# Kernel tuning notes

Measured on AMD Instinct MI355X. Metric: run time of the kernel, lower is better.

The kernel has to match this reference:

```python
import jax, jax.numpy as jnp
import numpy as np

DIM = 2048
N_HEADS = 16
N_KV = 4
HEAD_DIM = DIM // N_HEADS  # 128
B, S = 2, 2048
EPS = float(np.finfo(np.float32).eps)  # torch RMSNorm eps=None -> finfo eps


def _rotate_half(x):
    # interleaved-pair rotation: out[..., ::2] = -x[..., 1::2]; out[..., 1::2] = x[..., ::2]
    x2 = x.reshape(x.shape[:-1] + (HEAD_DIM // 2, 2))
    rot = jnp.stack([-x2[..., 1], x2[..., 0]], axis=-1)
    return rot.reshape(x.shape)


def _rmsnorm(x, w):
    var = jnp.mean(x * x, axis=-1, keepdims=True)
    return x * jax.lax.rsqrt(var + EPS) * w


def setup_inputs() -> dict:
    key = jax.random.key(0)
    ks = jax.random.split(key, 5)
    out_f = (N_HEADS + 2 * N_KV) * HEAD_DIM  # 3072
    return {
        "x": jax.random.normal(ks[0], (B, S, DIM), jnp.float32),
        "wqkv": jax.random.normal(ks[1], (out_f, DIM), jnp.float32) * (2.0 / (DIM + out_f)) ** 0.5,
        "wo": jax.random.normal(ks[2], (DIM, DIM), jnp.float32) * (1.0 / DIM) ** 0.5,
        "q_norm_w": jnp.ones((HEAD_DIM,), jnp.float32),
        "k_norm_w": jnp.ones((HEAD_DIM,), jnp.float32),
        "freqs_cos": jnp.cos(jax.random.normal(ks[3], (S, 1, HEAD_DIM), jnp.float32)),
        "freqs_sin": jnp.sin(jax.random.normal(ks[4], (S, 1, HEAD_DIM), jnp.float32)),
    }


def reference(x, wqkv, wo, q_norm_w, k_norm_w, freqs_cos, freqs_sin):
    b, s, _ = x.shape
    qkv = jnp.einsum("bsd,od->bso", x, wqkv)
    q_size = N_HEADS * HEAD_DIM
    kv_size = N_KV * HEAD_DIM
    xq = qkv[..., :q_size].reshape(b, s, N_HEADS, HEAD_DIM)
    xk = qkv[..., q_size:q_size + kv_size].reshape(b, s, N_KV, HEAD_DIM)
    xv = qkv[..., q_size + kv_size:].reshape(b, s, N_KV, HEAD_DIM)
    xq = _rmsnorm(xq, q_norm_w)
    xk = _rmsnorm(xk, k_norm_w)
    # RoPE (freqs broadcast over batch and heads)
    xq = xq * freqs_cos + _rotate_half(xq) * freqs_sin
    xk = xk * freqs_cos + _rotate_half(xk) * freqs_sin
    # GQA: group query heads per kv head instead of materializing repeats
    rep = N_HEADS // N_KV
    q = xq.transpose(0, 2, 1, 3).reshape(b, N_KV, rep, s, HEAD_DIM)
    k = xk.transpose(0, 2, 1, 3)  # [b, kv, s, d]
    v = xv.transpose(0, 2, 1, 3)
    scale = 1.0 / jnp.sqrt(jnp.asarray(HEAD_DIM, x.dtype))
    scores = jnp.einsum("bhgqd,bhkd->bhgqk", q, k) * scale
    probs = jax.nn.softmax(scores, axis=-1)
    attn = jnp.einsum("bhgqk,bhkd->bhgqd", probs, v)
    attn = attn.reshape(b, N_HEADS, s, HEAD_DIM).transpose(0, 2, 1, 3).reshape(b, s, DIM)
    return jnp.einsum("bsd,od->bso", attn, wo)
```

## Files before the change

### kernel.cpp

```cpp
#include <hip/hip_runtime.h>

typedef unsigned short u16;
typedef __bf16 bf16x8 __attribute__((ext_vector_type(8)));
typedef u16 u16x8 __attribute__((ext_vector_type(8)));
typedef float f32x4 __attribute__((ext_vector_type(4)));
typedef float f32x16 __attribute__((ext_vector_type(16)));

__device__ __forceinline__ u16 f2bf(float f) {
    unsigned u = __float_as_uint(f);
    return (u16)((u + 0x7fffu + ((u >> 16) & 1u)) >> 16);
}
__device__ __forceinline__ unsigned pk2(float a, float b) {
    return (unsigned)f2bf(a) | ((unsigned)f2bf(b) << 16);
}

__global__ void cvt_bf16(const float* __restrict__ src, u16* __restrict__ dst, int n4) {
    int i = blockIdx.x * 256 + threadIdx.x;
    if (i >= n4) return;
    float4 v = *(const float4*)(src + (size_t)i * 4);
    uint2 o; o.x = pk2(v.x, v.y); o.y = pk2(v.z, v.w);
    *(uint2*)(dst + (size_t)i * 4) = o;
}

__global__ __launch_bounds__(256)
void gemm_bt(const u16* __restrict__ A, const u16* __restrict__ B,
             float* __restrict__ C, int M, int N, int K) {
    __shared__ u16 As[128 * 32];
    __shared__ u16 Bs[128 * 32];
    const int tid = threadIdx.x;
    const int wave = tid >> 6, lane = tid & 63;
    const int quad = lane >> 4, l16 = lane & 15;
    const size_t bm = (size_t)blockIdx.y * 128;
    const size_t bn = (size_t)blockIdx.x * 128;
    const int wr = (wave >> 1) * 64;
    const int wc = (wave & 1) * 64;

    f32x4 acc[4][4] = {};

    const u16* Ab = A + bm * K;
    const u16* Bb = B + bn * K;
    const int strow = wave * 32 + (lane >> 2);
    const int stk = (lane & 3) * 8;

    for (int k0 = 0; k0 < K; k0 += 32) {
        __syncthreads();
#pragma unroll
        for (int c = 0; c < 2; ++c) {
            const u16* ga = Ab + (size_t)(strow + c * 16) * K + k0 + stk;
            const u16* gb = Bb + (size_t)(strow + c * 16) * K + k0 + stk;
            __builtin_amdgcn_global_load_lds(
                (__attribute__((address_space(1))) void*)ga,
                (__attribute__((address_space(3))) void*)&As[(wave * 32 + c * 16) * 32],
                16, 0, 0);
            __builtin_amdgcn_global_load_lds(
                (__attribute__((address_space(1))) void*)gb,
                (__attribute__((address_space(3))) void*)&Bs[(wave * 32 + c * 16) * 32],
                16, 0, 0);
        }
        __syncthreads();
        bf16x8 af[4], bfr[4];
#pragma unroll
        for (int mt = 0; mt < 4; ++mt)
            af[mt] = *(const bf16x8*)&As[(wr + mt * 16 + l16) * 32 + quad * 8];
#pragma unroll
        for (int nt = 0; nt < 4; ++nt)
            bfr[nt] = *(const bf16x8*)&Bs[(wc + nt * 16 + l16) * 32 + quad * 8];
#pragma unroll
        for (int mt = 0; mt < 4; ++mt)
#pragma unroll
            for (int nt = 0; nt < 4; ++nt)
                acc[mt][nt] = __builtin_amdgcn_mfma_f32_16x16x32_bf16(
                    af[mt], bfr[nt], acc[mt][nt], 0, 0, 0);
    }
#pragma unroll
    for (int mt = 0; mt < 4; ++mt)
#pragma unroll
        for (int nt = 0; nt < 4; ++nt)
#pragma unroll
            for (int r = 0; r < 4; ++r)
                C[(bm + wr + mt * 16 + quad * 4 + r) * (size_t)N + bn + wc + nt * 16 + l16] =
                    acc[mt][nt][r];
}

__global__ __launch_bounds__(256)
void normrope(const float* __restrict__ qkv, const float* __restrict__ qw,
              const float* __restrict__ kw, const float* __restrict__ fcos,
              const float* __restrict__ fsin, u16* __restrict__ qb, u16* __restrict__ kb) {
    int gw = blockIdx.x * 4 + (threadIdx.x >> 6);
    int lane = threadIdx.x & 63;
    int row = gw / 20;
    int task = gw - row * 20;
    int s = row & 2047;
    int b = row >> 11;
    const float* src;
    const float* w;
    u16* dst;
    float scl;
    if (task < 16) {
        src = qkv + (size_t)row * 3072 + task * 128;
        w = qw;
        dst = qb + ((size_t)(b * 16 + task) * 2048 + s) * 128;
        scl = 0.08838834764831845f * 1.4426950408889634f;
    } else {
        int kh = task - 16;
        src = qkv + (size_t)row * 3072 + 2048 + kh * 128;
        w = kw;
        dst = kb + ((size_t)(b * 4 + kh) * 2048 + s) * 128;
        scl = 1.0f;
    }
    float2 x = *(const float2*)(src + lane * 2);
    float ss = x.x * x.x + x.y * x.y;
#pragma unroll
    for (int off = 32; off >= 1; off >>= 1) ss += __shfl_xor(ss, off);
    float r = rsqrtf(ss * (1.0f / 128.0f) + 1.1920928955078125e-07f) * scl;
    float y0 = x.x * r * w[lane * 2];
    float y1 = x.y * r * w[lane * 2 + 1];
    float c0 = fcos[(size_t)s * 128 + lane * 2], c1 = fcos[(size_t)s * 128 + lane * 2 + 1];
    float s0 = fsin[(size_t)s * 128 + lane * 2], s1 = fsin[(size_t)s * 128 + lane * 2 + 1];
    dst[lane * 2]     = f2bf(y0 * c0 - y1 * s0);
    dst[lane * 2 + 1] = f2bf(y1 * c1 + y0 * s1);
}

__global__ __launch_bounds__(256)
void vtrans(const float* __restrict__ qkv, u16* __restrict__ vt) {
    __shared__ u16 tile[128 * 132];
    int blk = blockIdx.x;
    int kblk = blk & 15, kh = (blk >> 4) & 3, b = blk >> 6;
    int tid = threadIdx.x;
    const float* src = qkv + (size_t)(b * 2048 + kblk * 128) * 3072 + 2560 + kh * 128;
#pragma unroll
    for (int it = 0; it < 16; ++it) {
        int flat4 = tid + it * 256;
        int row = flat4 >> 5, c4 = flat4 & 31;
        float4 v = *(const float4*)(src + (size_t)row * 3072 + c4 * 4);
        u16* d = &tile[row * 132 + c4 * 4];
        d[0] = f2bf(v.x); d[1] = f2bf(v.y); d[2] = f2bf(v.z); d[3] = f2bf(v.w);
    }
    __syncthreads();
    int dd = tid >> 1, half = tid & 1;
    u16* dst = vt + ((size_t)(b * 4 + kh) * 128 + dd) * 2048 + kblk * 128 + half * 64;
#pragma unroll
    for (int k8 = 0; k8 < 8; ++k8) {
        u16x8 o;
#pragma unroll
        for (int j = 0; j < 8; ++j) o[j] = tile[(half * 64 + k8 * 8 + j) * 132 + dd];
        *(u16x8*)(dst + k8 * 8) = o;
    }
}

#define KBUF(c) ((c) * 8192)
#define VBUF(c) (16384 + (c) * 8192)
__global__ __launch_bounds__(256, 2)
void flash_attn(const u16* __restrict__ qb, const u16* __restrict__ kb,
                const u16* __restrict__ vt, u16* __restrict__ ab) {
    __shared__ u16 smem[32768];
    __shared__ float Llds[128];

    const int tid = threadIdx.x;
    const int wave = tid >> 6, lane = tid & 63;
    const int hf = lane >> 5, c32 = lane & 31;
    const int qt = blockIdx.x, hh = blockIdx.y, bb = blockIdx.z;
    const int kh = hh >> 2;

    const u16* Qbase = qb + (size_t)(bb * 16 + hh) * 2048 * 128;
    const u16* Kbase = kb + (size_t)(bb * 4 + kh) * 2048 * 128;
    const u16* Vbase = vt + (size_t)(bb * 4 + kh) * 128 * 2048;

    bf16x8 aq[8];
#pragma unroll
    for (int kq = 0; kq < 8; ++kq)
        aq[kq] = *(const bf16x8*)(Qbase +
            (size_t)(qt * 128 + wave * 32 + c32) * 128 + kq * 16 + hf * 8);

    f32x16 O[4] = {};
    float lacc = 0.f;

    const int st_key = tid >> 4, st_c16 = tid & 15;
    const int st_d = tid >> 3, st_c8 = tid & 7;

    u16x8 kreg[4], vreg[4];
#pragma unroll
    for (int it = 0; it < 4; ++it) {
        int key = st_key + it * 16, d = st_d + it * 32;
        kreg[it] = *(const u16x8*)(Kbase + (size_t)key * 128 + st_c16 * 8);
        vreg[it] = *(const u16x8*)(Vbase + (size_t)d * 2048 + st_c8 * 8);
    }
#pragma unroll
    for (int it = 0; it < 4; ++it) {
        int key = st_key + it * 16, d = st_d + it * 32;
        *(u16x8*)&smem[KBUF(0) + key * 128 + ((st_c16 ^ (key & 7)) * 8)] = kreg[it];
        *(u16x8*)&smem[VBUF(0) + d * 64 + ((st_c8 ^ (d & 7)) * 8)] = vreg[it];
    }
    __syncthreads();

    for (int kt = 0; kt < 32; ++kt) {
        const int cur = kt & 1, nxt = cur ^ 1;
        if (kt < 31) {
            const int key0n = (kt + 1) * 64;
#pragma unroll
            for (int it = 0; it < 4; ++it) {
                int key = st_key + it * 16, d = st_d + it * 32;
                kreg[it] = *(const u16x8*)(Kbase + (size_t)(key0n + key) * 128 + st_c16 * 8);
                vreg[it] = *(const u16x8*)(Vbase + (size_t)d * 2048 + key0n + st_c8 * 8);
            }
        }

        f32x16 sc[2] = {};
#pragma unroll
        for (int kq = 0; kq < 8; ++kq) {
#pragma unroll
            for (int mt = 0; mt < 2; ++mt) {
                bf16x8 kf = *(const bf16x8*)&smem[KBUF(cur) + (mt * 32 + c32) * 128 +
                                                 (((kq * 2 + hf) ^ (c32 & 7)) * 8)];
                sc[mt] = __builtin_amdgcn_mfma_f32_32x32x16_bf16(kf, aq[kq], sc[mt], 0, 0, 0);
            }
        }

        int pdw[2][8];
#pragma unroll
        for (int mt = 0; mt < 2; ++mt) {
            float p[16];
#pragma unroll
            for (int r = 0; r < 16; ++r) {
                p[r] = __builtin_amdgcn_exp2f(sc[mt][r]);
                lacc += p[r];
            }
#pragma unroll
            for (int i = 0; i < 8; ++i) pdw[mt][i] = (int)pk2(p[2 * i], p[2 * i + 1]);
        }

        if (kt < 31) {
#pragma unroll
            for (int it = 0; it < 4; ++it) {
                int key = st_key + it * 16, d = st_d + it * 32;
                *(u16x8*)&smem[KBUF(nxt) + key * 128 + ((st_c16 ^ (key & 7)) * 8)] = kreg[it];
                *(u16x8*)&smem[VBUF(nxt) + d * 64 + ((st_c8 ^ (d & 7)) * 8)] = vreg[it];
            }
        }

#pragma unroll
        for (int kc = 0; kc < 4; ++kc) {
            const int mt = kc >> 1, L = kc & 1;
            int s0 = hf ? pdw[mt][4 * L + 0] : pdw[mt][4 * L + 2];
            int s1 = hf ? pdw[mt][4 * L + 1] : pdw[mt][4 * L + 3];
            int r0 = __shfl_xor(s0, 32);
            int r1 = __shfl_xor(s1, 32);
            union { int i[4]; bf16x8 v; } u;
            u.i[0] = hf ? r0 : pdw[mt][4 * L + 0];
            u.i[1] = hf ? r1 : pdw[mt][4 * L + 1];
            u.i[2] = hf ? pdw[mt][4 * L + 2] : r0;
            u.i[3] = hf ? pdw[mt][4 * L + 3] : r1;
#pragma unroll
            for (int dt = 0; dt < 4; ++dt) {
                bf16x8 vf = *(const bf16x8*)&smem[VBUF(cur) + (dt * 32 + c32) * 64 +
                                                 (((kc * 2 + hf) ^ (c32 & 7)) * 8)];
                O[dt] = __builtin_amdgcn_mfma_f32_32x32x16_bf16(u.v, vf, O[dt], 0, 0, 0);
            }
        }
        __syncthreads();
    }

    float l = lacc + __shfl_xor(lacc, 32);
    if (hf == 0) Llds[wave * 32 + c32] = l;

    float inv[16];
#pragma unroll
    for (int r = 0; r < 16; ++r)
        inv[r] = __builtin_amdgcn_rcpf(Llds[wave * 32 + (r & 3) + 8 * (r >> 2) + 4 * hf]);

    u16* scr = &smem[wave * 32 * 136];
#pragma unroll
    for (int dt = 0; dt < 4; ++dt)
#pragma unroll
        for (int r = 0; r < 16; ++r) {
            int q_r = (r & 3) + 8 * (r >> 2) + 4 * hf;
            scr[q_r * 136 + dt * 32 + c32] = f2bf(O[dt][r] * inv[r]);
        }
#pragma unroll
    for (int it = 0; it < 8; ++it) {
        int f = it * 64 + lane;
        int row = f >> 4, c = f & 15;
        u16x8 v = *(const u16x8*)&scr[row * 136 + c * 8];
        int qg = qt * 128 + wave * 32 + row;
        *(u16x8*)(ab + ((size_t)(bb * 2048 + qg)) * 2048 + hh * 128 + c * 8) = v;
    }
}

extern "C" void kernel_launch(void* const* d_in, const int* in_sizes, int n_in,
                              void* d_out, int out_size, void* d_ws, size_t ws_size,
                              hipStream_t stream) {
    const float* x    = (const float*)d_in[0];
    const float* wqkv = (const float*)d_in[1];
    const float* wo   = (const float*)d_in[2];
    const float* qw   = (const float*)d_in[3];
    const float* kw   = (const float*)d_in[4];
    const float* fc   = (const float*)d_in[5];
    const float* fs   = (const float*)d_in[6];
    float* out = (float*)d_out;
    char* ws = (char*)d_ws;

    u16*   xb    = (u16*)(ws + 0);
    u16*   wqkvb = (u16*)(ws + 16777216);
    u16*   wob   = (u16*)(ws + 29360128);
    float* qkv   = (float*)(ws + 37748736);
    u16*   qb    = (u16*)(ws + 88080384);
    u16*   kb    = (u16*)(ws + 104857600);
    u16*   vt    = (u16*)(ws + 109051904);
    u16*   ab    = (u16*)(ws + 113246208);

    cvt_bf16<<<8192, 256, 0, stream>>>(x, xb, 2097152);
    cvt_bf16<<<6144, 256, 0, stream>>>(wqkv, wqkvb, 1572864);
    cvt_bf16<<<4096, 256, 0, stream>>>(wo, wob, 1048576);
    gemm_bt<<<dim3(24, 32), 256, 0, stream>>>(xb, wqkvb, qkv, 4096, 3072, 2048);
    normrope<<<20480, 256, 0, stream>>>(qkv, qw, kw, fc, fs, qb, kb);
    vtrans<<<128, 256, 0, stream>>>(qkv, vt);
    flash_attn<<<dim3(16, 16, 2), 256, 0, stream>>>(qb, kb, vt, ab);
    gemm_bt<<<dim3(16, 32), 256, 0, stream>>>(ab, wob, out, 4096, 2048, 2048);
}
```

Before: 361.3 us.

## Fuse RMSNorm, RoPE and V transpose into QKV GEMM epilogue; double-buffer GEMM

Result: faster. 333.3 us (-7.7%).

```diff
diff --git a/kernel.cpp b/kernel.cpp
--- a/kernel.cpp
+++ b/kernel.cpp
@@ -1,7 +1,9 @@
 #include <hip/hip_runtime.h>
+#include <hip/hip_bf16.h>
 
 typedef unsigned short u16;
 typedef __bf16 bf16x8 __attribute__((ext_vector_type(8)));
+typedef __bf16 bf16x4 __attribute__((ext_vector_type(4)));
 typedef u16 u16x8 __attribute__((ext_vector_type(8)));
 typedef float f32x4 __attribute__((ext_vector_type(4)));
 typedef float f32x16 __attribute__((ext_vector_type(16)));
@@ -10,68 +12,80 @@
     unsigned u = __float_as_uint(f);
     return (u16)((u + 0x7fffu + ((u >> 16) & 1u)) >> 16);
 }
-__device__ __forceinline__ unsigned pk2(float a, float b) {
-    return (unsigned)f2bf(a) | ((unsigned)f2bf(b) << 16);
+__device__ __forceinline__ unsigned pkbf2(float a, float b) {
+    __hip_bfloat162 h = __float22bfloat162_rn(make_float2(a, b));
+    return *(unsigned*)&h;
 }
 
 __global__ void cvt_bf16(const float* __restrict__ src, u16* __restrict__ dst, int n4) {
     int i = blockIdx.x * 256 + threadIdx.x;
     if (i >= n4) return;
     float4 v = *(const float4*)(src + (size_t)i * 4);
-    uint2 o; o.x = pk2(v.x, v.y); o.y = pk2(v.z, v.w);
+    uint2 o; o.x = pkbf2(v.x, v.y); o.y = pkbf2(v.z, v.w);
     *(uint2*)(dst + (size_t)i * 4) = o;
+}
+
+__device__ __forceinline__ void gemm_core(const u16* __restrict__ Ab,
+                                          const u16* __restrict__ Bb, int K,
+                                          f32x4 acc[4][4], int wave, int lane) {
+    __shared__ u16 As[2][128 * 32];
+    __shared__ u16 Bs[2][128 * 32];
+    const int quad = lane >> 4, l16 = lane & 15;
+    const int wr = (wave >> 1) * 64, wc = (wave & 1) * 64;
+    const int strow = lane >> 2;
+    const int stk = (lane & 3) * 8;
+
+    const u16* pa0 = Ab + (size_t)(wave * 32 + strow) * K + stk;
+    const u16* pa1 = pa0 + (size_t)16 * K;
+    const u16* pb0 = Bb + (size_t)(wave * 32 + strow) * K + stk;
+    const u16* pb1 = pb0 + (size_t)16 * K;
+    const int lrow0 = (wave * 32 + strow) * 32 + stk;
+    const int lrow1 = (wave * 32 + 16 + strow) * 32 + stk;
+
+    u16x8 a0 = *(const u16x8*)pa0, a1 = *(const u16x8*)pa1;
+    u16x8 b0 = *(const u16x8*)pb0, b1 = *(const u16x8*)pb1;
+    *(u16x8*)&As[0][lrow0] = a0; *(u16x8*)&As[0][lrow1] = a1;
+    *(u16x8*)&Bs[0][lrow0] = b0; *(u16x8*)&Bs[0][lrow1] = b1;
+    __syncthreads();
+
+    const int nk = K >> 5;
+    for (int kt = 0; kt < nk; ++kt) {
+        const int cur = kt & 1, nxt = cur ^ 1;
+        if (kt + 1 < nk) {
+            const int off = (kt + 1) * 32;
+            a0 = *(const u16x8*)(pa0 + off); a1 = *(const u16x8*)(pa1 + off);
+            b0 = *(const u16x8*)(pb0 + off); b1 = *(const u16x8*)(pb1 + off);
+        }
+        bf16x8 af[4], bfr[4];
+#pragma unroll
+        for (int mt = 0; mt < 4; ++mt)
+            af[mt] = *(const bf16x8*)&As[cur][(wr + mt * 16 + l16) * 32 + quad * 8];
+#pragma unroll
+        for (int nt = 0; nt < 4; ++nt)
+            bfr[nt] = *(const bf16x8*)&Bs[cur][(wc + nt * 16 + l16) * 32 + quad * 8];
+#pragma unroll
+        for (int mt = 0; mt < 4; ++mt)
+#pragma unroll
+            for (int nt = 0; nt < 4; ++nt)
+                acc[mt][nt] = __builtin_amdgcn_mfma_f32_16x16x32_bf16(
+                    af[mt], bfr[nt], acc[mt][nt], 0, 0, 0);
+        if (kt + 1 < nk) {
+            *(u16x8*)&As[nxt][lrow0] = a0; *(u16x8*)&As[nxt][lrow1] = a1;
+            *(u16x8*)&Bs[nxt][lrow0] = b0; *(u16x8*)&Bs[nxt][lrow1] = b1;
+        }
+        __syncthreads();
+    }
 }
 
 __global__ __launch_bounds__(256)
 void gemm_bt(const u16* __restrict__ A, const u16* __restrict__ B,
              float* __restrict__ C, int M, int N, int K) {
-    __shared__ u16 As[128 * 32];
-    __shared__ u16 Bs[128 * 32];
-    const int tid = threadIdx.x;
-    const int wave = tid >> 6, lane = tid & 63;
+    const int tid = threadIdx.x, wave = tid >> 6, lane = tid & 63;
     const int quad = lane >> 4, l16 = lane & 15;
-    const size_t bm = (size_t)blockIdx.y * 128;
-    const size_t bn = (size_t)blockIdx.x * 128;
-    const int wr = (wave >> 1) * 64;
-    const int wc = (wave & 1) * 64;
-
+    const int wr = (wave >> 1) * 64, wc = (wave & 1) * 64;
+    const size_t bm = (size_t)blockIdx.y * 128, bn = (size_t)blockIdx.x * 128;
     f32x4 acc[4][4] = {};
-
-    const u16* Ab = A + bm * K;
-    const u16* Bb = B + bn * K;
-    const int strow = wave * 32 + (lane >> 2);
-    const int stk = (lane & 3) * 8;
-
-    for (int k0 = 0; k0 < K; k0 += 32) {
-        __syncthreads();
-#pragma unroll
-        for (int c = 0; c < 2; ++c) {
-            const u16* ga = Ab + (size_t)(strow + c * 16) * K + k0 + stk;
-            const u16* gb = Bb + (size_t)(strow + c * 16) * K + k0 + stk;
-            __builtin_amdgcn_global_load_lds(
-                (__attribute__((address_space(1))) void*)ga,
-                (__attribute__((address_space(3))) void*)&As[(wave * 32 + c * 16) * 32],
-                16, 0, 0);
-            __builtin_amdgcn_global_load_lds(
-                (__attribute__((address_space(1))) void*)gb,
-                (__attribute__((address_space(3))) void*)&Bs[(wave * 32 + c * 16) * 32],
-                16, 0, 0);
-        }
-        __syncthreads();
-        bf16x8 af[4], bfr[4];
-#pragma unroll
-        for (int mt = 0; mt < 4; ++mt)
-            af[mt] = *(const bf16x8*)&As[(wr + mt * 16 + l16) * 32 + quad * 8];
-#pragma unroll
-        for (int nt = 0; nt < 4; ++nt)
-            bfr[nt] = *(const bf16x8*)&Bs[(wc + nt * 16 + l16) * 32 + quad * 8];
-#pragma unroll
-        for (int mt = 0; mt < 4; ++mt)
-#pragma unroll
-            for (int nt = 0; nt < 4; ++nt)
-                acc[mt][nt] = __builtin_amdgcn_mfma_f32_16x16x32_bf16(
-                    af[mt], bfr[nt], acc[mt][nt], 0, 0, 0);
-    }
+    gemm_core(A + bm * K, B + bn * K, K, acc, wave, lane);
 #pragma unroll
     for (int mt = 0; mt < 4; ++mt)
 #pragma unroll
@@ -83,68 +97,88 @@
 }
 
 __global__ __launch_bounds__(256)
-void normrope(const float* __restrict__ qkv, const float* __restrict__ qw,
-              const float* __restrict__ kw, const float* __restrict__ fcos,
-              const float* __restrict__ fsin, u16* __restrict__ qb, u16* __restrict__ kb) {
-    int gw = blockIdx.x * 4 + (threadIdx.x >> 6);
-    int lane = threadIdx.x & 63;
-    int row = gw / 20;
-    int task = gw - row * 20;
-    int s = row & 2047;
-    int b = row >> 11;
-    const float* src;
-    const float* w;
-    u16* dst;
-    float scl;
-    if (task < 16) {
-        src = qkv + (size_t)row * 3072 + task * 128;
-        w = qw;
-        dst = qb + ((size_t)(b * 16 + task) * 2048 + s) * 128;
-        scl = 0.08838834764831845f * 1.4426950408889634f;
-    } else {
-        int kh = task - 16;
-        src = qkv + (size_t)row * 3072 + 2048 + kh * 128;
-        w = kw;
-        dst = kb + ((size_t)(b * 4 + kh) * 2048 + s) * 128;
-        scl = 1.0f;
-    }
-    float2 x = *(const float2*)(src + lane * 2);
-    float ss = x.x * x.x + x.y * x.y;
-#pragma unroll
-    for (int off = 32; off >= 1; off >>= 1) ss += __shfl_xor(ss, off);
-    float r = rsqrtf(ss * (1.0f / 128.0f) + 1.1920928955078125e-07f) * scl;
-    float y0 = x.x * r * w[lane * 2];
-    float y1 = x.y * r * w[lane * 2 + 1];
-    float c0 = fcos[(size_t)s * 128 + lane * 2], c1 = fcos[(size_t)s * 128 + lane * 2 + 1];
-    float s0 = fsin[(size_t)s * 128 + lane * 2], s1 = fsin[(size_t)s * 128 + lane * 2 + 1];
-    dst[lane * 2]     = f2bf(y0 * c0 - y1 * s0);
-    dst[lane * 2 + 1] = f2bf(y1 * c1 + y0 * s1);
-}
-
-__global__ __launch_bounds__(256)
-void vtrans(const float* __restrict__ qkv, u16* __restrict__ vt) {
-    __shared__ u16 tile[128 * 132];
-    int blk = blockIdx.x;
-    int kblk = blk & 15, kh = (blk >> 4) & 3, b = blk >> 6;
-    int tid = threadIdx.x;
-    const float* src = qkv + (size_t)(b * 2048 + kblk * 128) * 3072 + 2560 + kh * 128;
-#pragma unroll
-    for (int it = 0; it < 16; ++it) {
-        int flat4 = tid + it * 256;
-        int row = flat4 >> 5, c4 = flat4 & 31;
-        float4 v = *(const float4*)(src + (size_t)row * 3072 + c4 * 4);
-        u16* d = &tile[row * 132 + c4 * 4];
-        d[0] = f2bf(v.x); d[1] = f2bf(v.y); d[2] = f2bf(v.z); d[3] = f2bf(v.w);
-    }
+void gemm_qkv(const u16* __restrict__ xb, const u16* __restrict__ wq,
+              const float* __restrict__ qw, const float* __restrict__ kw,
+              const float* __restrict__ fcos, const float* __restrict__ fsin,
+              u16* __restrict__ qb, u16* __restrict__ kb, u16* __restrict__ vt) {
+    const int tid = threadIdx.x, wave = tid >> 6, lane = tid & 63;
+    const int quad = lane >> 4, l16 = lane & 15;
+    const int wr = (wave >> 1) * 64, wc = (wave & 1) * 64;
+    const int tn = blockIdx.x, bmb = blockIdx.y;
+    f32x4 acc[4][4] = {};
+    gemm_core(xb + (size_t)bmb * 128 * 2048, wq + (size_t)tn * 128 * 2048, 2048,
+              acc, wave, lane);
+
+    const int b = bmb >> 4;
+    const int sbase = (bmb & 15) * 128 + wr;
+
+    if (tn >= 20) {
+        const int kv = tn - 20;
+        u16* base = vt + (size_t)(b * 4 + kv) * 128 * 2048;
+#pragma unroll
+        for (int mt = 0; mt < 4; ++mt) {
+            int s0 = sbase + mt * 16 + quad * 4;
+#pragma unroll
+            for (int nt = 0; nt < 4; ++nt) {
+                int col = wc + nt * 16 + l16;
+                bf16x4 pv;
+#pragma unroll
+                for (int r = 0; r < 4; ++r) pv[r] = (__bf16)acc[mt][nt][r];
+                *(bf16x4*)(base + (size_t)col * 2048 + s0) = pv;
+            }
+        }
+        return;
+    }
+
+    __shared__ float red[2][128];
+    float ssq[4][4];
+#pragma unroll
+    for (int mt = 0; mt < 4; ++mt)
+#pragma unroll
+        for (int r = 0; r < 4; ++r) {
+            float t = 0.f;
+#pragma unroll
+            for (int nt = 0; nt < 4; ++nt) t += acc[mt][nt][r] * acc[mt][nt][r];
+#pragma unroll
+            for (int off = 1; off <= 8; off <<= 1) t += __shfl_xor(t, off);
+            ssq[mt][r] = t;
+        }
+    if (l16 == 0)
+#pragma unroll
+        for (int mt = 0; mt < 4; ++mt)
+#pragma unroll
+            for (int r = 0; r < 4; ++r)
+                red[wave & 1][wr + mt * 16 + quad * 4 + r] = ssq[mt][r];
     __syncthreads();
-    int dd = tid >> 1, half = tid & 1;
-    u16* dst = vt + ((size_t)(b * 4 + kh) * 128 + dd) * 2048 + kblk * 128 + half * 64;
-#pragma unroll
-    for (int k8 = 0; k8 < 8; ++k8) {
-        u16x8 o;
-#pragma unroll
-        for (int j = 0; j < 8; ++j) o[j] = tile[(half * 64 + k8 * 8 + j) * 132 + dd];
-        *(u16x8*)(dst + k8 * 8) = o;
+
+    const float qscl = (tn < 16) ? 0.08838834764831845f * 1.4426950408889634f : 1.0f;
+    const float* wp = (tn < 16) ? qw : kw;
+    float wcol[4];
+#pragma unroll
+    for (int nt = 0; nt < 4; ++nt) wcol[nt] = wp[wc + nt * 16 + l16];
+    u16* dstbase = (tn < 16) ? qb + (size_t)(b * 16 + tn) * 2048 * 128
+                             : kb + (size_t)(b * 4 + (tn - 16)) * 2048 * 128;
+    const float sgn = (l16 & 1) ? 1.f : -1.f;
+
+#pragma unroll
+    for (int mt = 0; mt < 4; ++mt) {
+#pragma unroll
+        for (int r = 0; r < 4; ++r) {
+            int row = wr + mt * 16 + quad * 4 + r;
+            float var = (red[0][row] + red[1][row]) * (1.0f / 128.0f);
+            float rms = rsqrtf(var + 1.1920928955078125e-07f) * qscl;
+            int s = sbase + mt * 16 + quad * 4 + r;
+            const float* fc = fcos + (size_t)s * 128 + wc;
+            const float* fn = fsin + (size_t)s * 128 + wc;
+            u16* drow = dstbase + (size_t)s * 128 + wc;
+#pragma unroll
+            for (int nt = 0; nt < 4; ++nt) {
+                float y = acc[mt][nt][r] * rms * wcol[nt];
+                float yp = __shfl_xor(y, 1);
+                float o = y * fc[nt * 16 + l16] + sgn * yp * fn[nt * 16 + l16];
+                drow[nt * 16 + l16] = f2bf(o);
+            }
+        }
     }
 }
 
@@ -226,7 +260,7 @@
                 lacc += p[r];
             }
 #pragma unroll
-            for (int i = 0; i < 8; ++i) pdw[mt][i] = (int)pk2(p[2 * i], p[2 * i + 1]);
+            for (int i = 0; i < 8; ++i) pdw[mt][i] = (int)pkbf2(p[2 * i], p[2 * i + 1]);
         }
 
         if (kt < 31) {
@@ -299,21 +333,18 @@
     float* out = (float*)d_out;
     char* ws = (char*)d_ws;
 
-    u16*   xb    = (u16*)(ws + 0);
-    u16*   wqkvb = (u16*)(ws + 16777216);
-    u16*   wob   = (u16*)(ws + 29360128);
-    float* qkv   = (float*)(ws + 37748736);
-    u16*   qb    = (u16*)(ws + 88080384);
-    u16*   kb    = (u16*)(ws + 104857600);
-    u16*   vt    = (u16*)(ws + 109051904);
-    u16*   ab    = (u16*)(ws + 113246208);
+    u16* xb    = (u16*)(ws + 0);
+    u16* wqkvb = (u16*)(ws + 16777216);
+    u16* wob   = (u16*)(ws + 29360128);
+    u16* qb    = (u16*)(ws + 37748736);
+    u16* kb    = (u16*)(ws + 54525952);
+    u16* vt    = (u16*)(ws + 58720256);
+    u16* ab    = (u16*)(ws + 62914560);
 
     cvt_bf16<<<8192, 256, 0, stream>>>(x, xb, 2097152);
     cvt_bf16<<<6144, 256, 0, stream>>>(wqkv, wqkvb, 1572864);
     cvt_bf16<<<4096, 256, 0, stream>>>(wo, wob, 1048576);
-    gemm_bt<<<dim3(24, 32), 256, 0, stream>>>(xb, wqkvb, qkv, 4096, 3072, 2048);
-    normrope<<<20480, 256, 0, stream>>>(qkv, qw, kw, fc, fs, qb, kb);
-    vtrans<<<128, 256, 0, stream>>>(qkv, vt);
+    gemm_qkv<<<dim3(24, 32), 256, 0, stream>>>(xb, wqkvb, qw, kw, fc, fs, qb, kb, vt);
     flash_attn<<<dim3(16, 16, 2), 256, 0, stream>>>(qb, kb, vt, ab);
     gemm_bt<<<dim3(16, 32), 256, 0, stream>>>(ab, wob, out, 4096, 2048, 2048);
 }
```
